# Performance work log

Measured on AMD Instinct MI355X. Metric: run time of the kernel, lower is better.

Reference implementation:

```python
import jax, jax.numpy as jnp
import numpy as np

R = 32
EPS = 0.0
BN_EPS = 1e-5


def _voxelize(features, idx):
    # features: [C, N], idx: [N] int32 flat voxel index in [0, R^3)
    V = R * R * R
    pts = features.T  # [N, C]
    sums = jax.ops.segment_sum(pts, idx, num_segments=V)          # [V, C]
    cnts = jax.ops.segment_sum(jnp.ones_like(idx, jnp.float32), idx, num_segments=V)  # [V]
    avg = sums / jnp.maximum(cnts, 1.0)[:, None]
    mx = jax.ops.segment_max(pts, idx, num_segments=V)            # [V, C], -inf for empty
    mx = jnp.where(cnts[:, None] > 0, mx, 0.0)
    return avg, mx, cnts


def reference(features, coords, conv_w, conv_b, bn_gamma, bn_beta, bn_mean, bn_var):
    B, C, N = features.shape
    # --- coordinate normalization (coords detached in original) ---
    nc = coords - jnp.mean(coords, axis=2, keepdims=True)          # [B,3,N]
    norms = jnp.linalg.norm(nc, axis=1, keepdims=True)             # [B,1,N]
    denom = jnp.max(norms, axis=2, keepdims=True) * 2.0 + EPS      # [B,1,1]
    nc = nc / denom + 0.5
    nc = jnp.clip(nc * R, 0.0, R - 1)                              # [B,3,N]
    vox = jnp.round(nc).astype(jnp.int32)                          # [B,3,N]
    idx = vox[:, 0] * (R * R) + vox[:, 1] * R + vox[:, 2]          # [B,N]
    # --- dual scatter reduction (avg + max) per batch ---
    avg, mx, _ = jax.vmap(_voxelize)(features, idx)                # [B, V, C] each
    fea = jnp.concatenate([mx, avg], axis=-1)                      # [B, V, 2C]
    # --- 1x1 Conv3d == channel matmul ---
    y = jnp.einsum('bvc,oc->bvo', fea, conv_w) + conv_b            # [B, V, C]
    # --- BatchNorm3d (eval mode) ---
    y = (y - bn_mean) * (bn_gamma / jnp.sqrt(bn_var + BN_EPS)) + bn_beta
    # --- Swish ---
    y = y * jax.nn.sigmoid(y)
    out = jnp.transpose(y, (0, 2, 1)).reshape(B, C, R, R, R)
    return out, nc


def setup_inputs() -> dict:
    key = jax.random.key(0)
    ks = jax.random.split(key, 8)
    B, C, N = 8, 240, 16384
    return {
        'features': jax.random.normal(ks[0], (B, C, N), jnp.float32),
        'coords': jax.random.normal(ks[1], (B, 3, N), jnp.float32),
        'conv_w': jax.random.normal(ks[2], (C, 2 * C), jnp.float32) * 0.05,
        'conv_b': jax.random.normal(ks[3], (C,), jnp.float32) * 0.05,
        'bn_gamma': jnp.ones((C,), jnp.float32),
        'bn_beta': jnp.zeros((C,), jnp.float32),
        'bn_mean': jnp.zeros((C,), jnp.float32),
        'bn_var': jax.random.uniform(ks[4], (C,), jnp.float32, 0.5, 1.5),
    }
```

## Files before the change

### kernel.cpp

```cpp
#include <hip/hip_runtime.h>
#include <math.h>

#define RR 32
#define V 32768
#define C 240
#define N 16384
#define B 8
#define K2C 480
#define GZ 16
#define NGRP 2048
#define FPAD 488
#define EBUF 512

typedef __attribute__((ext_vector_type(8))) short bf16x8;
typedef __attribute__((ext_vector_type(4))) float f32x4;

__device__ __forceinline__ unsigned short f2bf(float x) {
    unsigned u = __float_as_uint(x);
    u += 0x7fffu + ((u >> 16) & 1u);
    return (unsigned short)(u >> 16);
}

__global__ __launch_bounds__(256) void prep_kernel(const float* __restrict__ feat,
                                                   unsigned short* __restrict__ featT,
                                                   const float* __restrict__ coords,
                                                   float* __restrict__ stats,
                                                   int* __restrict__ hist,
                                                   int* __restrict__ wlcnt,
                                                   const float* __restrict__ w,
                                                   unsigned short* __restrict__ w_bf) {
    __shared__ float t[C][33];
    int blk = blockIdx.x;
    int tid = threadIdx.x;
    if (blk < 4096) {
        int bx = blk & 511, b = blk >> 9;
        int n0 = bx * 32;
        int l = tid;
        const float* fb = feat + (size_t)b * C * N;
        unsigned short* fTb = featT + (size_t)b * N * C;
        int nl = l & 31, cs = l >> 5;
#pragma unroll
        for (int p = 0; p < 30; ++p) {
            int c = p * 8 + cs;
            t[c][nl] = fb[(size_t)c * N + n0 + nl];
        }
        __syncthreads();
        int ci = l & 127;
        int nh = l >> 7;
#pragma unroll
        for (int p = 0; p < 16; ++p) {
            int n = 2 * p + nh;
            if (ci < 120) {
                unsigned lo = f2bf(t[2 * ci][n]);
                unsigned hi = f2bf(t[2 * ci + 1][n]);
                *(unsigned*)&fTb[(size_t)(n0 + n) * C + 2 * ci] = lo | (hi << 16);
            }
        }
        return;
    }
    if (blk < 4352) {
        int tt = (blk - 4096) * 256 + tid;
        int4 z4 = {0, 0, 0, 0};
        ((int4*)hist)[tt] = z4;
        if (tt < 57600) {
            unsigned lo = f2bf(w[2 * tt]);
            unsigned hi = f2bf(w[2 * tt + 1]);
            ((unsigned*)w_bf)[tt] = lo | (hi << 16);
        }
        if (tt < 2 * B) wlcnt[tt] = 0;
        return;
    }
    int b = blk - 4352;
    const float* cb = coords + (size_t)b * 3 * N;
    __shared__ float red[256];
    float m[3];
    for (int d = 0; d < 3; ++d) {
        float s = 0.f;
        for (int n = tid; n < N; n += 256) s += cb[d * N + n];
        red[tid] = s; __syncthreads();
        for (int w2 = 128; w2 > 0; w2 >>= 1) { if (tid < w2) red[tid] += red[tid + w2]; __syncthreads(); }
        m[d] = red[0] / (float)N;
        __syncthreads();
    }
    float mx = 0.f;
    for (int n = tid; n < N; n += 256) {
        float dx = cb[0 * N + n] - m[0];
        float dy = cb[1 * N + n] - m[1];
        float dz = cb[2 * N + n] - m[2];
        mx = fmaxf(mx, dx * dx + dy * dy + dz * dz);
    }
    red[tid] = mx; __syncthreads();
    for (int w2 = 128; w2 > 0; w2 >>= 1) { if (tid < w2) red[tid] = fmaxf(red[tid], red[tid + w2]); __syncthreads(); }
    if (tid == 0) {
        stats[b * 4 + 0] = m[0];
        stats[b * 4 + 1] = m[1];
        stats[b * 4 + 2] = m[2];
        stats[b * 4 + 3] = 2.f * sqrtf(red[0]);
    }
}

__global__ __launch_bounds__(256) void nc_idx_kernel(const float* __restrict__ coords,
                                                     const float* __restrict__ stats,
                                                     float* __restrict__ nc_out,
                                                     int* __restrict__ idxbuf,
                                                     int* __restrict__ hist) {
    int t = blockIdx.x * 256 + threadIdx.x;
    int b = t >> 14;
    int n = t & (N - 1);
    float denom = stats[b * 4 + 3];
    int v[3];
#pragma unroll
    for (int d = 0; d < 3; ++d) {
        float x = coords[((size_t)b * 3 + d) * N + n];
        float t0 = (x - stats[b * 4 + d]) / denom + 0.5f;
        t0 = t0 * (float)RR;
        t0 = fminf(fmaxf(t0, 0.f), (float)(RR - 1));
        nc_out[((size_t)b * 3 + d) * N + n] = t0;
        v[d] = (int)rintf(t0);
    }
    int iv = v[0] * (RR * RR) + v[1] * RR + v[2];
    idxbuf[t] = iv;
    atomicAdd(hist + b * V + iv, 1);
}

__global__ __launch_bounds__(1024) void prefix_kernel(const int* __restrict__ hist,
                                                      int* __restrict__ starts,
                                                      int* __restrict__ cursor,
                                                      int* __restrict__ wl,
                                                      int* __restrict__ wlcnt) {
    __shared__ int part[1024];
    int b = blockIdx.x, t = threadIdx.x;
    int base = b * V + t * 32;
    const int4* hp = (const int4*)(hist + base);
    int4 h[8];
#pragma unroll
    for (int j = 0; j < 8; ++j) h[j] = hp[j];
    int pcA = h[0].x + h[0].y + h[0].z + h[0].w + h[1].x + h[1].y + h[1].z + h[1].w
            + h[2].x + h[2].y + h[2].z + h[2].w + h[3].x + h[3].y + h[3].z + h[3].w;
    int pcB = h[4].x + h[4].y + h[4].z + h[4].w + h[5].x + h[5].y + h[5].z + h[5].w
            + h[6].x + h[6].y + h[6].z + h[6].w + h[7].x + h[7].y + h[7].z + h[7].w;
    int s = pcA + pcB;
    if (pcA > 0) { int p = atomicAdd(wlcnt + b, 1); wl[b * NGRP + p] = 2 * t; }
    if (pcB > 0) { int p = atomicAdd(wlcnt + b, 1); wl[b * NGRP + p] = 2 * t + 1; }
    if (pcA == 0 && pcB == 0) { int q = atomicAdd(wlcnt + B + b, 1); wl[b * NGRP + NGRP - 1 - q] = (2 * t) | 0x10000; }
    else if (pcA == 0)        { int q = atomicAdd(wlcnt + B + b, 1); wl[b * NGRP + NGRP - 1 - q] = 2 * t; }
    else if (pcB == 0)        { int q = atomicAdd(wlcnt + B + b, 1); wl[b * NGRP + NGRP - 1 - q] = 2 * t + 1; }
    part[t] = s; __syncthreads();
    for (int off = 1; off < 1024; off <<= 1) {
        int x = (t >= off) ? part[t - off] : 0;
        __syncthreads();
        part[t] += x;
        __syncthreads();
    }
    int run = part[t] - s;
    int4* sp = (int4*)(starts + base);
    int4* cp = (int4*)(cursor + base);
#pragma unroll
    for (int j = 0; j < 8; ++j) {
        int4 o;
        o.x = run; run += h[j].x;
        o.y = run; run += h[j].y;
        o.z = run; run += h[j].z;
        o.w = run; run += h[j].w;
        sp[j] = o; cp[j] = o;
    }
}

__global__ __launch_bounds__(256) void plist_kernel(const int* __restrict__ idxbuf,
                                                    int* __restrict__ cursor,
                                                    int* __restrict__ ptlist) {
    int t = blockIdx.x * 256 + threadIdx.x;
    int b = t >> 14;
    int n = t & (N - 1);
    int iv = idxbuf[t];
    int pos = atomicAdd(cursor + b * V + iv, 1);
    ptlist[(b << 14) + pos] = (n << 5) | (iv & 31);
}

#define PREFETCH(U, Z0, Z1, basei)                                          \
    {                                                                       \
        Z0 = 0u; Z1 = 0u;                                                   \
        _Pragma("unroll")                                                   \
        for (int j = 0; j < 16; ++j) {                                      \
            int idx = basei + j; idx = (idx < mm) ? idx : mm - 1;           \
            int e = ebuf[idx];                                              \
            U[j] = fT[(size_t)(e >> 5) * C + c];                            \
            unsigned zz = (unsigned)(e & 15);                               \
            if (j < 8) Z0 |= zz << (4 * j); else Z1 |= zz << (4 * (j - 8)); \
        }                                                                   \
    }

#define PROCESS(U, Z0, Z1, basei)                                           \
    {                                                                       \
        _Pragma("unroll")                                                   \
        for (int j = 0; j < 16; ++j) {                                      \
            if (basei + j < mm) {                                           \
                int zj = (int)(((j < 8 ? Z0 : Z1) >> (4 * (j & 7))) & 15u); \
                if (zj != curz) {                                           \
                    if (curz >= 0) {                                        \
                        fea_s[curz][c] = f2bf(mx0);                         \
                        fea_s[curz][C + c] = f2bf(s0 * rcp_s[curz]);        \
                    }                                                       \
                    curz = zj; s0 = 0.f; mx0 = -INFINITY;                   \
                }                                                           \
                float f = __uint_as_float(((unsigned)U[j]) << 16);          \
                s0 += f; mx0 = fmaxf(mx0, f);                               \
            }                                                               \
        }                                                                   \
    }

__global__ __launch_bounds__(256) void column_kernel(
    const unsigned short* __restrict__ featT,
    const int* __restrict__ ptlist,
    const int* __restrict__ starts,
    const int* __restrict__ hist,
    const unsigned short* __restrict__ w_bf,
    const float* __restrict__ cbias, const float* __restrict__ gamma,
    const float* __restrict__ beta, const float* __restrict__ mean,
    const float* __restrict__ var,
    const int* __restrict__ wl, const int* __restrict__ wlcnt,
    float* __restrict__ out) {
    const int bx = blockIdx.x, b = blockIdx.y;
    const int nw = wlcnt[b];
    const int ntot = nw + wlcnt[B + b];
    if (bx >= ntot) return;
    const bool isfill = (bx >= nw);
    const int wle = isfill ? wl[b * NGRP + NGRP - 1 - (bx - nw)] : wl[b * NGRP + bx];
    const int tid = threadIdx.x;
    float* outb = out + (size_t)b * C * V;

    __shared__ float A_s[C], B_s[C], y0_s[C], rcp_s[GZ];
    __shared__ unsigned short fea_s[GZ][FPAD];
    __shared__ int cnt_s[GZ];
    __shared__ int ebuf[EBUF];

    const int g = wle & 0xffff;
    const int v0 = g * GZ;

    if (tid < C) {
        float sc = gamma[tid] * rsqrtf(var[tid] + 1e-5f);
        A_s[tid] = sc;
        float b0 = (cbias[tid] - mean[tid]) * sc + beta[tid];
        B_s[tid] = b0;
        y0_s[tid] = b0 / (1.f + __expf(-b0));
    }
    if (!isfill && tid < GZ) {
        int c0 = hist[b * V + v0 + tid];
        cnt_s[tid] = c0;
        rcp_s[tid] = 1.f / (float)max(c0, 1);
    }
    __syncthreads();

    if (isfill) {
        if (wle >> 16) {
            for (int i = tid; i < C * 8; i += 256) {
                int o = i >> 3, q = i & 7;
                float y = y0_s[o];
                float4 f4 = {y, y, y, y};
                *(float4*)&outb[(size_t)o * V + v0 + q * 4] = f4;
            }
        } else {
            for (int i = tid; i < C * 4; i += 256) {
                int o = i >> 2, q = i & 3;
                float y = y0_s[o];
                float4 f4 = {y, y, y, y};
                *(float4*)&outb[(size_t)o * V + v0 + q * 4] = f4;
            }
        }
        return;
    }

    int pc = 0;
#pragma unroll
    for (int z = 0; z < GZ; ++z) pc += cnt_s[z];

    for (int i = tid; i < GZ * FPAD / 2; i += 256) ((unsigned*)fea_s)[i] = 0u;

    const int c = tid;
    const bool act = tid < C;
    const int pos = starts[b * V + v0];
    const int* pl = ptlist + (b << 14) + pos;
    const unsigned short* fT = featT + (size_t)b * N * C;

    float s0 = 0.f, mx0 = -INFINITY;
    int curz = -1;
    for (int base = 0; base < pc; base += EBUF) {
        int mm = min(EBUF, pc - base);
        __syncthreads();
        for (int i = tid; i < mm; i += 256) ebuf[i] = pl[base + i];
        __syncthreads();
        if (act) {
            unsigned short uA[16], uB[16];
            unsigned zA0 = 0, zA1 = 0, zB0 = 0, zB1 = 0;
            PREFETCH(uA, zA0, zA1, 0);
            for (int i0 = 0; i0 < mm; i0 += 32) {
                if (i0 + 16 < mm) PREFETCH(uB, zB0, zB1, i0 + 16);
                PROCESS(uA, zA0, zA1, i0);
                if (i0 + 32 < mm) PREFETCH(uA, zA0, zA1, i0 + 32);
                PROCESS(uB, zB0, zB1, i0 + 16);
            }
        }
    }
    if (act && curz >= 0) {
        fea_s[curz][c] = f2bf(mx0);
        fea_s[curz][C + c] = f2bf(s0 * rcp_s[curz]);
    }
    __syncthreads();

    const int lane = tid & 63, wave = tid >> 6;
    const int mcnt = (wave == 3) ? 3 : 4;
    const int zl = lane & 15;
    const int koff = (lane >> 4) * 8;

    f32x4 acc[4];
#pragma unroll
    for (int i = 0; i < 4; ++i) acc[i] = (f32x4){0.f, 0.f, 0.f, 0.f};

#pragma unroll
    for (int kc = 0; kc < 15; ++kc) {
        const int kg = kc * 32 + koff;
        bf16x8 bfr = *(const bf16x8*)&fea_s[zl][kg];
        const unsigned short* wp = w_bf + (size_t)(wave * 64 + zl) * K2C + kg;
#pragma unroll
        for (int mt = 0; mt < 4; ++mt) {
            if (mt < mcnt) {
                bf16x8 afr = *(const bf16x8*)(wp + (size_t)mt * 16 * K2C);
                acc[mt] = __builtin_amdgcn_mfma_f32_16x16x32_bf16(afr, bfr, acc[mt], 0, 0, 0);
            }
        }
    }

    const int vv = v0 + zl;
    const int rbase = (lane >> 4) * 4;
#pragma unroll
    for (int mt = 0; mt < 4; ++mt) {
        if (mt < mcnt) {
#pragma unroll
            for (int r = 0; r < 4; ++r) {
                int o = (wave * 4 + mt) * 16 + rbase + r;
                float y = acc[mt][r] * A_s[o] + B_s[o];
                y = y / (1.f + __expf(-y));
                outb[(size_t)o * V + vv] = y;
            }
        }
    }
}

extern "C" void kernel_launch(void* const* d_in, const int* in_sizes, int n_in,
                              void* d_out, int out_size, void* d_ws, size_t ws_size,
                              hipStream_t stream) {
    const float* features = (const float*)d_in[0];
    const float* coords   = (const float*)d_in[1];
    const float* conv_w   = (const float*)d_in[2];
    const float* conv_b   = (const float*)d_in[3];
    const float* gamma    = (const float*)d_in[4];
    const float* beta     = (const float*)d_in[5];
    const float* mean     = (const float*)d_in[6];
    const float* var      = (const float*)d_in[7];

    float* out    = (float*)d_out;
    float* nc_out = out + (size_t)B * C * V;

    char* ws = (char*)d_ws;
    size_t off = 0;
    auto carve = [&](size_t bytes) { char* p = ws + off; off += (bytes + 255) & ~(size_t)255; return p; };
    int*            hist   = (int*)carve((size_t)B * V * 4);
    float*          stats  = (float*)carve(B * 4 * 4);
    int*            idxbuf = (int*)carve((size_t)B * N * 4);
    int*            starts = (int*)carve((size_t)B * V * 4);
    int*            cursor = (int*)carve((size_t)B * V * 4);
    int*            ptlist = (int*)carve((size_t)B * N * 4);
    int*            wl     = (int*)carve((size_t)B * NGRP * 4);
    int*            wlcnt  = (int*)carve((size_t)2 * B * 4);
    unsigned short* w_bf   = (unsigned short*)carve((size_t)C * K2C * 2);
    unsigned short* featT  = (unsigned short*)carve((size_t)B * N * C * 2);
    (void)off;

    prep_kernel<<<4360, 256, 0, stream>>>(features, featT, coords, stats, hist, wlcnt, conv_w, w_bf);
    nc_idx_kernel<<<(B * N) / 256, 256, 0, stream>>>(coords, stats, nc_out, idxbuf, hist);
    prefix_kernel<<<B, 1024, 0, stream>>>(hist, starts, cursor, wl, wlcnt);
    plist_kernel<<<(B * N) / 256, 256, 0, stream>>>(idxbuf, cursor, ptlist);
    column_kernel<<<dim3(NGRP, B), 256, 0, stream>>>(
        featT, ptlist, starts, hist, w_bf,
        conv_b, gamma, beta, mean, var, wl, wlcnt, out);
    (void)in_sizes; (void)n_in; (void)out_size;
}
```

Before: 580.5 us.

## Process two voxel groups per block to reuse weight fragments across MFMAs

Each non-fill block now handles two 16-voxel work groups: it gathers both into a doubled shared feature tile, then runs the MFMA loop with each loaded weight fragment applied to both groups. This halves the number of weight loads per voxel and the per-block setup cost (BN constants, launch). It adds shared memory use and accumulator registers and serializes the gather of two groups within one block. Launch bounds are also raised to request 4 blocks per CU. The grid size appears unchanged, so the surplus blocks exit early.

```diff
diff --git a/kernel.cpp b/kernel.cpp
--- a/kernel.cpp
+++ b/kernel.cpp
@@ -198,8 +198,8 @@
                 int zj = (int)(((j < 8 ? Z0 : Z1) >> (4 * (j & 7))) & 15u); \
                 if (zj != curz) {                                           \
                     if (curz >= 0) {                                        \
-                        fea_s[curz][c] = f2bf(mx0);                         \
-                        fea_s[curz][C + c] = f2bf(s0 * rcp_s[curz]);        \
+                        fea_s[rb + curz][c] = f2bf(mx0);                    \
+                        fea_s[rb + curz][C + c] = f2bf(s0 * rcp_s[rb + curz]); \
                     }                                                       \
                     curz = zj; s0 = 0.f; mx0 = -INFINITY;                   \
                 }                                                           \
@@ -209,7 +209,7 @@
         }                                                                   \
     }
 
-__global__ __launch_bounds__(256) void column_kernel(
+__global__ __launch_bounds__(256, 4) void column_kernel(
     const unsigned short* __restrict__ featT,
     const int* __restrict__ ptlist,
     const int* __restrict__ starts,
@@ -222,20 +222,29 @@
     float* __restrict__ out) {
     const int bx = blockIdx.x, b = blockIdx.y;
     const int nw = wlcnt[b];
-    const int ntot = nw + wlcnt[B + b];
+    const int npair = (nw + 1) >> 1;
+    const int ntot = npair + wlcnt[B + b];
     if (bx >= ntot) return;
-    const bool isfill = (bx >= nw);
-    const int wle = isfill ? wl[b * NGRP + NGRP - 1 - (bx - nw)] : wl[b * NGRP + bx];
+    const bool isfill = (bx >= npair);
     const int tid = threadIdx.x;
     float* outb = out + (size_t)b * C * V;
 
-    __shared__ float A_s[C], B_s[C], y0_s[C], rcp_s[GZ];
-    __shared__ unsigned short fea_s[GZ][FPAD];
-    __shared__ int cnt_s[GZ];
+    __shared__ float A_s[C], B_s[C], y0_s[C], rcp_s[2 * GZ];
+    __shared__ unsigned short fea_s[2 * GZ][FPAD];
+    __shared__ int cnt_s[2 * GZ];
     __shared__ int ebuf[EBUF];
 
-    const int g = wle & 0xffff;
-    const int v0 = g * GZ;
+    int wle0, wle1 = 0;
+    bool has1 = false;
+    if (isfill) {
+        wle0 = wl[b * NGRP + NGRP - 1 - (bx - npair)];
+    } else {
+        wle0 = wl[b * NGRP + 2 * bx];
+        has1 = (2 * bx + 1) < nw;
+        wle1 = has1 ? wl[b * NGRP + 2 * bx + 1] : wle0;
+    }
+    const int v00 = (wle0 & 0xffff) * GZ;
+    const int v01 = (wle1 & 0xffff) * GZ;
 
     if (tid < C) {
         float sc = gamma[tid] * rsqrtf(var[tid] + 1e-5f);
@@ -244,66 +253,74 @@
         B_s[tid] = b0;
         y0_s[tid] = b0 / (1.f + __expf(-b0));
     }
-    if (!isfill && tid < GZ) {
-        int c0 = hist[b * V + v0 + tid];
+    if (!isfill && tid < 2 * GZ) {
+        int c0;
+        if (tid < GZ) c0 = hist[b * V + v00 + tid];
+        else          c0 = has1 ? hist[b * V + v01 + (tid - GZ)] : 0;
         cnt_s[tid] = c0;
         rcp_s[tid] = 1.f / (float)max(c0, 1);
     }
     __syncthreads();
 
     if (isfill) {
-        if (wle >> 16) {
+        if (wle0 >> 16) {
             for (int i = tid; i < C * 8; i += 256) {
                 int o = i >> 3, q = i & 7;
                 float y = y0_s[o];
                 float4 f4 = {y, y, y, y};
-                *(float4*)&outb[(size_t)o * V + v0 + q * 4] = f4;
+                *(float4*)&outb[(size_t)o * V + v00 + q * 4] = f4;
             }
         } else {
             for (int i = tid; i < C * 4; i += 256) {
                 int o = i >> 2, q = i & 3;
                 float y = y0_s[o];
                 float4 f4 = {y, y, y, y};
-                *(float4*)&outb[(size_t)o * V + v0 + q * 4] = f4;
+                *(float4*)&outb[(size_t)o * V + v00 + q * 4] = f4;
             }
         }
         return;
     }
 
-    int pc = 0;
-#pragma unroll
-    for (int z = 0; z < GZ; ++z) pc += cnt_s[z];
-
-    for (int i = tid; i < GZ * FPAD / 2; i += 256) ((unsigned*)fea_s)[i] = 0u;
+    int pc0 = 0, pc1 = 0;
+#pragma unroll
+    for (int z = 0; z < GZ; ++z) { pc0 += cnt_s[z]; pc1 += cnt_s[GZ + z]; }
+
+    for (int i = tid; i < 2 * GZ * FPAD / 2; i += 256) ((unsigned*)fea_s)[i] = 0u;
 
     const int c = tid;
     const bool act = tid < C;
-    const int pos = starts[b * V + v0];
-    const int* pl = ptlist + (b << 14) + pos;
     const unsigned short* fT = featT + (size_t)b * N * C;
 
-    float s0 = 0.f, mx0 = -INFINITY;
-    int curz = -1;
-    for (int base = 0; base < pc; base += EBUF) {
-        int mm = min(EBUF, pc - base);
-        __syncthreads();
-        for (int i = tid; i < mm; i += 256) ebuf[i] = pl[base + i];
-        __syncthreads();
-        if (act) {
-            unsigned short uA[16], uB[16];
-            unsigned zA0 = 0, zA1 = 0, zB0 = 0, zB1 = 0;
-            PREFETCH(uA, zA0, zA1, 0);
-            for (int i0 = 0; i0 < mm; i0 += 32) {
-                if (i0 + 16 < mm) PREFETCH(uB, zB0, zB1, i0 + 16);
-                PROCESS(uA, zA0, zA1, i0);
-                if (i0 + 32 < mm) PREFETCH(uA, zA0, zA1, i0 + 32);
-                PROCESS(uB, zB0, zB1, i0 + 16);
-            }
-        }
-    }
-    if (act && curz >= 0) {
-        fea_s[curz][c] = f2bf(mx0);
-        fea_s[curz][C + c] = f2bf(s0 * rcp_s[curz]);
+#pragma unroll 1
+    for (int grp = 0; grp < 2; ++grp) {
+        const int pc = grp ? pc1 : pc0;
+        if (pc == 0) continue;
+        const int rb = grp << 4;
+        const int pos = starts[b * V + (grp ? v01 : v00)];
+        const int* pl = ptlist + (b << 14) + pos;
+        float s0 = 0.f, mx0 = -INFINITY;
+        int curz = -1;
+        for (int base = 0; base < pc; base += EBUF) {
+            int mm = min(EBUF, pc - base);
+            __syncthreads();
+            for (int i = tid; i < mm; i += 256) ebuf[i] = pl[base + i];
+            __syncthreads();
+            if (act) {
+                unsigned short uA[16], uB[16];
+                unsigned zA0 = 0, zA1 = 0, zB0 = 0, zB1 = 0;
+                PREFETCH(uA, zA0, zA1, 0);
+                for (int i0 = 0; i0 < mm; i0 += 32) {
+                    if (i0 + 16 < mm) PREFETCH(uB, zB0, zB1, i0 + 16);
+                    PROCESS(uA, zA0, zA1, i0);
+                    if (i0 + 32 < mm) PREFETCH(uA, zA0, zA1, i0 + 32);
+                    PROCESS(uB, zB0, zB1, i0 + 16);
+                }
+            }
+        }
+        if (act && curz >= 0) {
+            fea_s[rb + curz][c] = f2bf(mx0);
+            fea_s[rb + curz][C + c] = f2bf(s0 * rcp_s[rb + curz]);
+        }
     }
     __syncthreads();
 
@@ -311,36 +328,43 @@
     const int mcnt = (wave == 3) ? 3 : 4;
     const int zl = lane & 15;
     const int koff = (lane >> 4) * 8;
-
-    f32x4 acc[4];
-#pragma unroll
-    for (int i = 0; i < 4; ++i) acc[i] = (f32x4){0.f, 0.f, 0.f, 0.f};
+    const int rbase = (lane >> 4) * 4;
+
+    f32x4 acc0[4], acc1[4];
+#pragma unroll
+    for (int i = 0; i < 4; ++i) { acc0[i] = (f32x4){0.f, 0.f, 0.f, 0.f}; acc1[i] = (f32x4){0.f, 0.f, 0.f, 0.f}; }
 
 #pragma unroll
     for (int kc = 0; kc < 15; ++kc) {
         const int kg = kc * 32 + koff;
-        bf16x8 bfr = *(const bf16x8*)&fea_s[zl][kg];
+        bf16x8 bfr0 = *(const bf16x8*)&fea_s[zl][kg];
+        bf16x8 bfr1 = *(const bf16x8*)&fea_s[GZ + zl][kg];
         const unsigned short* wp = w_bf + (size_t)(wave * 64 + zl) * K2C + kg;
 #pragma unroll
         for (int mt = 0; mt < 4; ++mt) {
             if (mt < mcnt) {
                 bf16x8 afr = *(const bf16x8*)(wp + (size_t)mt * 16 * K2C);
-                acc[mt] = __builtin_amdgcn_mfma_f32_16x16x32_bf16(afr, bfr, acc[mt], 0, 0, 0);
-            }
-        }
-    }
-
-    const int vv = v0 + zl;
-    const int rbase = (lane >> 4) * 4;
+                acc0[mt] = __builtin_amdgcn_mfma_f32_16x16x32_bf16(afr, bfr0, acc0[mt], 0, 0, 0);
+                acc1[mt] = __builtin_amdgcn_mfma_f32_16x16x32_bf16(afr, bfr1, acc1[mt], 0, 0, 0);
+            }
+        }
+    }
+
+    const int vv0 = v00 + zl, vv1 = v01 + zl;
 #pragma unroll
     for (int mt = 0; mt < 4; ++mt) {
         if (mt < mcnt) {
 #pragma unroll
             for (int r = 0; r < 4; ++r) {
                 int o = (wave * 4 + mt) * 16 + rbase + r;
-                float y = acc[mt][r] * A_s[o] + B_s[o];
+                float y = acc0[mt][r] * A_s[o] + B_s[o];
                 y = y / (1.f + __expf(-y));
-                outb[(size_t)o * V + vv] = y;
+                outb[(size_t)o * V + vv0] = y;
+                if (has1) {
+                    float y1 = acc1[mt][r] * A_s[o] + B_s[o];
+                    y1 = y1 / (1.f + __expf(-y1));
+                    outb[(size_t)o * V + vv1] = y1;
+                }
             }
         }
     }
```

After: 565.4 us. 2.6% less time.
